# Optimization experiments

Measured on AMD Instinct MI355X. Metric: run time of the kernel, lower is better.

Reference implementation:

```python
import jax, jax.numpy as jnp
import numpy as np

D = 9  # nodefeat_n1 = 3 (resnet feat) + 6 (pos)


def _lstm_scan(x, Wih, Whh, bih, bhh, reverse=False):
    # x: [T, B, D] -> hidden states [T, B, D]; torch gate order i,f,g,o
    B = x.shape[1]
    def step(carry, xt):
        h, c = carry
        g = xt @ Wih.T + bih + h @ Whh.T + bhh
        i = jax.nn.sigmoid(g[:, :D])
        f = jax.nn.sigmoid(g[:, D:2*D])
        gg = jnp.tanh(g[:, 2*D:3*D])
        o = jax.nn.sigmoid(g[:, 3*D:])
        c = f * c + i * gg
        h = o * jnp.tanh(c)
        return (h, c), h
    init = (jnp.zeros((B, D), x.dtype), jnp.zeros((B, D), x.dtype))
    _, hs = jax.lax.scan(step, init, x, reverse=reverse)
    return hs


def _forward(nodes_feature, pos, attmat, msg_W, msg_b, gru_Wih, gru_Whh, gru_bih, gru_bhh,
             ro1_W, ro1_b, ro2_W, ro2_b, lf_Wih, lf_Whh, lf_bih, lf_bhh,
             lb_Wih, lb_Whh, lb_bih, lb_bhh, lr1_W, lr1_b, lr2_W, lr2_b, num_rec):
    node_feat = jnp.concatenate([nodes_feature, pos], axis=-1)  # [N,T,M,D]
    N, T, M, _ = node_feat.shape
    # valid_node_num = num_rec[b, 0] in the original code
    valid = (jnp.arange(M)[None, :] < num_rec[:, 0:1]).astype(node_feat.dtype)  # [N,M]
    att = attmat * valid[:, None, None, :]  # zero out invalid source nodes q
    src = node_feat  # message sources (h_w)
    hv = node_feat   # GRU hidden (h_v)
    hidden = node_feat
    for _ in range(2):  # iterN = 2 message-passing rounds
        msg = src @ msg_W.T + msg_b                    # [N,T,M,D] message_fc
        m = jnp.einsum('btnq,btqd->btnd', att, msg)    # attention-weighted sum over q
        # single-step GRU cell (torch gate order r,z,n)
        gx = m @ gru_Wih.T + gru_bih
        gh = hv @ gru_Whh.T + gru_bhh
        r = jax.nn.sigmoid(gx[..., :D] + gh[..., :D])
        z = jax.nn.sigmoid(gx[..., D:2*D] + gh[..., D:2*D])
        n = jnp.tanh(gx[..., 2*D:] + r * gh[..., 2*D:])
        h_new = (1.0 - z) * n + z * hv
        hidden = h_new * valid[:, None, :, None]       # invalid nodes never updated -> stay zero
        src = hidden
        hv = hidden
    vmask = valid[:, None, :, None]
    # per-frame readout (pred_label0)
    p0 = jax.nn.relu(hidden @ ro1_W.T + ro1_b) @ ro2_W.T + ro2_b
    pred_label0 = p0 * vmask
    # bidirectional LSTM over time, batched over (batch, node)
    x = hidden.transpose(1, 0, 2, 3).reshape(T, N * M, D)  # [T, N*M, D]
    hf = _lstm_scan(x, lf_Wih, lf_Whh, lf_bih, lf_bhh, reverse=False)
    hb = _lstm_scan(x, lb_Wih, lb_Whh, lb_bih, lb_bhh, reverse=True)
    out = jnp.concatenate([hf, hb], axis=-1).reshape(T, N, M, 2 * D).transpose(1, 0, 2, 3)
    p = jax.nn.relu(out @ lr1_W.T + lr1_b) @ lr2_W.T + lr2_b
    pred_label = p * vmask
    return pred_label, pred_label0


def setup_inputs() -> dict:
    key = jax.random.key(0)
    ks = jax.random.split(key, 32)
    N, T, M = 8192, 20, 6
    def u(k, shape, fan_in):
        s = 1.0 / np.sqrt(fan_in).astype(np.float32)
        return jax.random.uniform(k, shape, jnp.float32, -s, s)
    return {
        "nodes_feature": jax.random.normal(ks[0], (N, T, M, 3), jnp.float32),
        "pos": jax.random.normal(ks[1], (N, T, M, 6), jnp.float32),
        "attmat": jax.random.uniform(ks[2], (N, T, M, M), jnp.float32),
        "msg_W": u(ks[3], (D, D), D), "msg_b": u(ks[4], (D,), D),
        "gru_Wih": u(ks[5], (3 * D, D), D), "gru_Whh": u(ks[6], (3 * D, D), D),
        "gru_bih": u(ks[7], (3 * D,), D), "gru_bhh": u(ks[8], (3 * D,), D),
        "ro1_W": u(ks[9], (D, D), D), "ro1_b": u(ks[10], (D,), D),
        "ro2_W": u(ks[11], (7, D), D), "ro2_b": u(ks[12], (7,), D),
        "lf_Wih": u(ks[13], (4 * D, D), D), "lf_Whh": u(ks[14], (4 * D, D), D),
        "lf_bih": u(ks[15], (4 * D,), D), "lf_bhh": u(ks[16], (4 * D,), D),
        "lb_Wih": u(ks[17], (4 * D, D), D), "lb_Whh": u(ks[18], (4 * D, D), D),
        "lb_bih": u(ks[19], (4 * D,), D), "lb_bhh": u(ks[20], (4 * D,), D),
        "lr1_W": u(ks[21], (D, 2 * D), 2 * D), "lr1_b": u(ks[22], (D,), 2 * D),
        "lr2_W": u(ks[23], (7, D), D), "lr2_b": u(ks[24], (7,), D),
        "num_rec": jax.random.randint(ks[25], (N, T), 1, M + 1),
    }


def reference(nodes_feature, pos, attmat, msg_W, msg_b, gru_Wih, gru_Whh, gru_bih, gru_bhh,
              ro1_W, ro1_b, ro2_W, ro2_b, lf_Wih, lf_Whh, lf_bih, lf_bhh,
              lb_Wih, lb_Whh, lb_bih, lb_bhh, lr1_W, lr1_b, lr2_W, lr2_b, num_rec):
    return _forward(nodes_feature, pos, attmat, msg_W, msg_b, gru_Wih, gru_Whh, gru_bih, gru_bhh,
                    ro1_W, ro1_b, ro2_W, ro2_b, lf_Wih, lf_Whh, lf_bih, lf_bhh,
                    lb_Wih, lb_Whh, lb_bih, lb_bhh, lr1_W, lr1_b, lr2_W, lr2_b, num_rec)
```

## Files before the change

kernel.cpp:

```cpp
#include <hip/hip_runtime.h>

#define N_    8192
#define T_    20
#define M_    6
#define D_    9
#define NM_   (N_*M_)
#define NT_   (N_*T_)
#define NTM7_ (N_*T_*M_*7)

#define LOG2E 1.44269504088896f

typedef __attribute__((ext_vector_type(2))) float v2f;

__device__ __forceinline__ float sigm(float x){
    return __builtin_amdgcn_rcpf(1.f + __builtin_amdgcn_exp2f(-LOG2E * x));
}
__device__ __forceinline__ float tanh_(float x){
    return fmaf(2.f, __builtin_amdgcn_rcpf(1.f + __builtin_amdgcn_exp2f(-2.f*LOG2E * x)), -1.f);
}
__device__ __forceinline__ float shfl_(float v, int src){ return __shfl(v, src, 64); }
__device__ __forceinline__ v2f splat(float s){ return (v2f){s, s}; }
__device__ __forceinline__ v2f shfl2(v2f v, int src){
    v2f r; r.x = __shfl(v.x, src, 64); r.y = __shfl(v.y, src, 64); return r;
}
__device__ __forceinline__ v2f sigm2(v2f x){ v2f r; r.x = sigm(x.x); r.y = sigm(x.y); return r; }
__device__ __forceinline__ v2f tanh2(v2f x){ v2f r; r.x = tanh_(x.x); r.y = tanh_(x.y); return r; }
__device__ __forceinline__ v2f relu2(v2f x){ v2f r; r.x = fmaxf(x.x,0.f); r.y = fmaxf(x.y,0.f); return r; }

__global__ __launch_bounds__(256) void k_gnn(
    const float* __restrict__ nf,
    const float* __restrict__ pos,
    const float* __restrict__ am,
    const float* __restrict__ msgW, const float* __restrict__ msgb,
    const float* __restrict__ gWih, const float* __restrict__ gWhh,
    const float* __restrict__ gbih, const float* __restrict__ gbhh,
    const float* __restrict__ ro1W, const float* __restrict__ ro1b,
    const float* __restrict__ ro2W, const float* __restrict__ ro2b,
    const int*   __restrict__ numrec,
    float* __restrict__ hid,
    float* __restrict__ out0)
{
    const int lane = threadIdx.x & 63;
    const int wib  = threadIdx.x >> 6;
    const int g    = lane / 6;
    const int i    = lane - g * 6;
    const int gbase = g * 6;
    const bool lactive = (lane < 60);

    const int wbase = (blockIdx.x * 4 + wib) * 20;
    const int ntA = wbase + g;
    const int ntB = wbase + 10 + g;
    const int nA = ntA / T_, tA = ntA - nA * T_;
    const int nB = ntB / T_, tB = ntB - nB * T_;

    v2f s[D_];
    {
        const float* pA = nf + (size_t)ntA * 18 + i * 3;
        const float* pB = nf + (size_t)ntB * 18 + i * 3;
        #pragma unroll
        for (int k = 0; k < 3; ++k) { s[k].x = pA[k]; s[k].y = pB[k]; }
    }
    {
        const float* pA = pos + (size_t)ntA * 36 + i * 6;
        const float* pB = pos + (size_t)ntB * 36 + i * 6;
        #pragma unroll
        for (int k = 0; k < 6; ++k) { s[3+k].x = pA[k]; s[3+k].y = pB[k]; }
    }
    v2f attr[M_];
    {
        const float* pA = am + (size_t)ntA * 36 + i * 6;
        const float* pB = am + (size_t)ntB * 36 + i * 6;
        #pragma unroll
        for (int q = 0; q < M_; ++q) { attr[q].x = pA[q]; attr[q].y = pB[q]; }
    }
    const int nrA = numrec[nA * T_];
    const int nrB = numrec[nB * T_];
    #pragma unroll
    for (int q = 0; q < M_; ++q) {
        attr[q].x *= (q < nrA) ? 1.f : 0.f;
        attr[q].y *= (q < nrB) ? 1.f : 0.f;
    }
    v2f vmi; vmi.x = (i < nrA) ? 1.f : 0.f; vmi.y = (i < nrB) ? 1.f : 0.f;

    #pragma unroll
    for (int it = 0; it < 2; ++it) {
        v2f msg[D_];
        #pragma unroll
        for (int d = 0; d < D_; ++d) {
            v2f a = splat(msgb[d]);
            #pragma unroll
            for (int k = 0; k < D_; ++k) a += s[k] * msgW[d*9 + k];
            msg[d] = a;
        }
        v2f mm[D_];
        #pragma unroll
        for (int d = 0; d < D_; ++d) {
            v2f a = splat(0.f);
            #pragma unroll
            for (int q = 0; q < M_; ++q) a += attr[q] * shfl2(msg[d], gbase + q);
            mm[d] = a;
        }
        v2f grz[18], gxn[9], ghn[9];
        #pragma unroll
        for (int j = 0; j < 18; ++j) {
            v2f a = splat(gbih[j] + gbhh[j]);
            #pragma unroll
            for (int k = 0; k < D_; ++k) {
                a += mm[k] * gWih[j*9 + k];
                a += s[k]  * gWhh[j*9 + k];
            }
            grz[j] = a;
        }
        #pragma unroll
        for (int j = 0; j < 9; ++j) {
            v2f ax = splat(gbih[18 + j]), ah = splat(gbhh[18 + j]);
            #pragma unroll
            for (int k = 0; k < D_; ++k) {
                ax += mm[k] * gWih[(18 + j)*9 + k];
                ah += s[k]  * gWhh[(18 + j)*9 + k];
            }
            gxn[j] = ax; ghn[j] = ah;
        }
        #pragma unroll
        for (int d = 0; d < D_; ++d) {
            v2f r  = sigm2(grz[d]);
            v2f z  = sigm2(grz[9 + d]);
            v2f nn = tanh2(gxn[d] + r * ghn[d]);
            s[d] = vmi * ((splat(1.f) - z) * nn + z * s[d]);
        }
    }

    if (lactive) {
        float* hpA = hid + (size_t)(nA * M_ + i) * (T_ * D_) + tA * D_;
        float* hpB = hid + (size_t)(nB * M_ + i) * (T_ * D_) + tB * D_;
        #pragma unroll
        for (int d = 0; d < D_; ++d) { hpA[d] = s[d].x; hpB[d] = s[d].y; }
    }

    v2f q9[D_];
    #pragma unroll
    for (int d = 0; d < D_; ++d) {
        v2f a = splat(ro1b[d]);
        #pragma unroll
        for (int k = 0; k < D_; ++k) a += s[k] * ro1W[d*9 + k];
        q9[d] = relu2(a);
    }
    if (lactive) {
        float* opA = out0 + (size_t)ntA * 42 + i * 7;
        float* opB = out0 + (size_t)ntB * 42 + i * 7;
        #pragma unroll
        for (int j = 0; j < 7; ++j) {
            v2f a = splat(ro2b[j]);
            #pragma unroll
            for (int k = 0; k < D_; ++k) a += q9[k] * ro2W[j*9 + k];
            a *= vmi;
            opA[j] = a.x; opB[j] = a.y;
        }
    }
}

#define CPB 14

__global__ __launch_bounds__(128) void k_lstm(
    const float* __restrict__ hid,
    const float* __restrict__ fWih, const float* __restrict__ fWhh,
    const float* __restrict__ fbih, const float* __restrict__ fbhh,
    const float* __restrict__ bWih, const float* __restrict__ bWhh,
    const float* __restrict__ bbih, const float* __restrict__ bbhh,
    const float* __restrict__ lr1W, const float* __restrict__ lr1b,
    const float* __restrict__ lr2W, const float* __restrict__ lr2b,
    const int*   __restrict__ numrec,
    float* __restrict__ out)
{
    __shared__ float hst[16 * 404];
    __shared__ float hxs[16 * 20];

    const int lane = threadIdx.x & 63;
    const int wib  = threadIdx.x >> 6;
    const int grp0 = lane / 9;
    const int d    = lane - grp0 * 9;
    const int row  = wib * 8 + grp0;
    const int grp  = (grp0 < 7) ? grp0 : 6;

    bool active = (lane < 63);
    int ci = blockIdx.x * CPB + wib * 7 + grp;
    active = active && (ci < NM_);
    const int nm = active ? ci : 0;

    const float* xb = hid + (size_t)nm * (T_ * D_);
    const int crow = row * 20;
    const int hrow = row * 404;

    {
        float wxi[9], wxf[9], wxg[9], wxo[9], whi[9], whf[9], whg[9], who[9];
        #pragma unroll
        for (int k = 0; k < 9; ++k) {
            wxi[k] = fWih[(d     )*9 + k];  whi[k] = fWhh[(d     )*9 + k];
            wxf[k] = fWih[(9  + d)*9 + k];  whf[k] = fWhh[(9  + d)*9 + k];
            wxg[k] = fWih[(18 + d)*9 + k];  whg[k] = fWhh[(18 + d)*9 + k];
            wxo[k] = fWih[(27 + d)*9 + k];  who[k] = fWhh[(27 + d)*9 + k];
        }
        const float bi = fbih[d]      + fbhh[d];
        const float bf = fbih[9 + d]  + fbhh[9 + d];
        const float bg = fbih[18 + d] + fbhh[18 + d];
        const float bo = fbih[27 + d] + fbhh[27 + d];

        hxs[crow + 2*d] = 0.f;
        float h = 0.f, c = 0.f;
        for (int t = 0; t < T_; ++t) {
            hxs[crow + 2*d + 1] = xb[t*9 + d];
            float gi = bi, gf = bf, gg = bg, go = bo;
            #pragma unroll
            for (int j = 0; j < 8; j += 2) {
                float4 v = *(const float4*)&hxs[crow + 2*j];
                gi = fmaf(v.x, whi[j], fmaf(v.y, wxi[j], gi));
                gf = fmaf(v.x, whf[j], fmaf(v.y, wxf[j], gf));
                gg = fmaf(v.x, whg[j], fmaf(v.y, wxg[j], gg));
                go = fmaf(v.x, who[j], fmaf(v.y, wxo[j], go));
                gi = fmaf(v.z, whi[j+1], fmaf(v.w, wxi[j+1], gi));
                gf = fmaf(v.z, whf[j+1], fmaf(v.w, wxf[j+1], gf));
                gg = fmaf(v.z, whg[j+1], fmaf(v.w, wxg[j+1], gg));
                go = fmaf(v.z, who[j+1], fmaf(v.w, wxo[j+1], go));
            }
            {
                float2 v = *(const float2*)&hxs[crow + 16];
                gi = fmaf(v.x, whi[8], fmaf(v.y, wxi[8], gi));
                gf = fmaf(v.x, whf[8], fmaf(v.y, wxf[8], gf));
                gg = fmaf(v.x, whg[8], fmaf(v.y, wxg[8], gg));
                go = fmaf(v.x, who[8], fmaf(v.y, wxo[8], go));
            }
            c = sigm(gf) * c + sigm(gi) * tanh_(gg);
            h = sigm(go) * tanh_(c);
            hst[hrow + t*20 + d] = h;
            hxs[crow + 2*d] = h;
        }
    }

    {
        float wxi[9], wxf[9], wxg[9], wxo[9], whi[9], whf[9], whg[9], who[9];
        #pragma unroll
        for (int k = 0; k < 9; ++k) {
            wxi[k] = bWih[(d     )*9 + k];  whi[k] = bWhh[(d     )*9 + k];
            wxf[k] = bWih[(9  + d)*9 + k];  whf[k] = bWhh[(9  + d)*9 + k];
            wxg[k] = bWih[(18 + d)*9 + k];  whg[k] = bWhh[(18 + d)*9 + k];
            wxo[k] = bWih[(27 + d)*9 + k];  who[k] = bWhh[(27 + d)*9 + k];
        }
        const float bi = bbih[d]      + bbhh[d];
        const float bf = bbih[9 + d]  + bbhh[9 + d];
        const float bg = bbih[18 + d] + bbhh[18 + d];
        const float bo = bbih[27 + d] + bbhh[27 + d];

        hxs[crow + 2*d] = 0.f;
        float h = 0.f, c = 0.f;
        for (int tt = T_ - 1; tt >= 0; --tt) {
            hxs[crow + 2*d + 1] = xb[tt*9 + d];
            float gi = bi, gf = bf, gg = bg, go = bo;
            #pragma unroll
            for (int j = 0; j < 8; j += 2) {
                float4 v = *(const float4*)&hxs[crow + 2*j];
                gi = fmaf(v.x, whi[j], fmaf(v.y, wxi[j], gi));
                gf = fmaf(v.x, whf[j], fmaf(v.y, wxf[j], gf));
                gg = fmaf(v.x, whg[j], fmaf(v.y, wxg[j], gg));
                go = fmaf(v.x, who[j], fmaf(v.y, wxo[j], go));
                gi = fmaf(v.z, whi[j+1], fmaf(v.w, wxi[j+1], gi));
                gf = fmaf(v.z, whf[j+1], fmaf(v.w, wxf[j+1], gf));
                gg = fmaf(v.z, whg[j+1], fmaf(v.w, wxg[j+1], gg));
                go = fmaf(v.z, who[j+1], fmaf(v.w, wxo[j+1], go));
            }
            {
                float2 v = *(const float2*)&hxs[crow + 16];
                gi = fmaf(v.x, whi[8], fmaf(v.y, wxi[8], gi));
                gf = fmaf(v.x, whf[8], fmaf(v.y, wxf[8], gf));
                gg = fmaf(v.x, whg[8], fmaf(v.y, wxg[8], gg));
                go = fmaf(v.x, who[8], fmaf(v.y, wxo[8], go));
            }
            c = sigm(gf) * c + sigm(gi) * tanh_(gg);
            h = sigm(go) * tanh_(c);
            hst[hrow + tt*20 + 10 + d] = h;
            hxs[crow + 2*d] = h;
        }
    }

    #pragma unroll 1
    for (int rr = 0; rr < 3; ++rr) {
        const int item = rr * 64 + lane;
        if (item >= 140) break;
        const int ch = item / 20;
        const int t  = item - ch * 20;
        const int ci2 = blockIdx.x * CPB + wib * 7 + ch;
        if (ci2 >= NM_) continue;
        const int base = (wib * 8 + ch) * 404 + t * 20;

        float hf[9], hb[9];
        #pragma unroll
        for (int j = 0; j < 4; ++j) {
            float2 a = *(const float2*)&hst[base + 2*j];
            hf[2*j] = a.x; hf[2*j+1] = a.y;
            float2 b = *(const float2*)&hst[base + 10 + 2*j];
            hb[2*j] = b.x; hb[2*j+1] = b.y;
        }
        hf[8] = hst[base + 8];
        hb[8] = hst[base + 18];

        const int n2 = ci2 / M_;
        const int m2 = ci2 - n2 * M_;
        const float vi = (m2 < numrec[n2 * T_]) ? 1.f : 0.f;

        float q[9];
        #pragma unroll
        for (int dd = 0; dd < 9; ++dd) {
            float a = lr1b[dd];
            #pragma unroll
            for (int k = 0; k < 9; ++k) a = fmaf(hf[k], lr1W[dd*18 + k], a);
            #pragma unroll
            for (int k = 0; k < 9; ++k) a = fmaf(hb[k], lr1W[dd*18 + 9 + k], a);
            q[dd] = fmaxf(a, 0.f);
        }
        float* op = out + (size_t)((n2 * T_ + t) * M_ + m2) * 7;
        #pragma unroll
        for (int j = 0; j < 7; ++j) {
            float a = lr2b[j];
            #pragma unroll
            for (int k = 0; k < 9; ++k) a = fmaf(q[k], lr2W[j*9 + k], a);
            op[j] = a * vi;
        }
    }
}

extern "C" void kernel_launch(void* const* d_in, const int* in_sizes, int n_in,
                              void* d_out, int out_size, void* d_ws, size_t ws_size,
                              hipStream_t stream) {
    const float* nf    = (const float*)d_in[0];
    const float* pos   = (const float*)d_in[1];
    const float* am    = (const float*)d_in[2];
    const float* msgW  = (const float*)d_in[3];
    const float* msgb  = (const float*)d_in[4];
    const float* gWih  = (const float*)d_in[5];
    const float* gWhh  = (const float*)d_in[6];
    const float* gbih  = (const float*)d_in[7];
    const float* gbhh  = (const float*)d_in[8];
    const float* ro1W  = (const float*)d_in[9];
    const float* ro1b  = (const float*)d_in[10];
    const float* ro2W  = (const float*)d_in[11];
    const float* ro2b  = (const float*)d_in[12];
    const float* lfWih = (const float*)d_in[13];
    const float* lfWhh = (const float*)d_in[14];
    const float* lfbih = (const float*)d_in[15];
    const float* lfbhh = (const float*)d_in[16];
    const float* lbWih = (const float*)d_in[17];
    const float* lbWhh = (const float*)d_in[18];
    const float* lbbih = (const float*)d_in[19];
    const float* lbbhh = (const float*)d_in[20];
    const float* lr1W  = (const float*)d_in[21];
    const float* lr1b  = (const float*)d_in[22];
    const float* lr2W  = (const float*)d_in[23];
    const float* lr2b  = (const float*)d_in[24];
    const int* numrec  = (const int*)d_in[25];

    float* hid = (float*)d_ws;

    float* outp = (float*)d_out;
    float* out0 = (float*)d_out + NTM7_;

    k_gnn <<<NT_ / 80, 256, 0, stream>>>(nf, pos, am, msgW, msgb, gWih, gWhh,
                                         gbih, gbhh, ro1W, ro1b, ro2W, ro2b,
                                         numrec, hid, out0);
    const int lgrid = (NM_ + CPB - 1) / CPB;
    k_lstm<<<lgrid, 128, 0, stream>>>(hid, lfWih, lfWhh, lfbih, lfbhh,
                                      lbWih, lbWhh, lbbih, lbbhh,
                                      lr1W, lr1b, lr2W, lr2b, numrec, outp);
}
```

Measured before the change: 323.2 us.

## Exchange GNN messages via LDS instead of wave shuffles, one-wave blocks

Messages are now written to a shared-memory buffer and read back as float4 rows, where each lane used to gather neighbour messages with 12 cross-lane shuffles per feature. Blocks shrink to a single wave, so no block-level barrier is needed, and the grid is enlarged to keep the same coverage. The pos and attention loads are widened to float2, and the inactive lanes 60-63 are clamped to index 0. The aim is to replace many ds_bpermute operations with a few LDS writes and vector reads, at the cost of LDS traffic and smaller blocks.

```diff
diff --git a/kernel.cpp b/kernel.cpp
--- a/kernel.cpp
+++ b/kernel.cpp
@@ -18,16 +18,12 @@
 __device__ __forceinline__ float tanh_(float x){
     return fmaf(2.f, __builtin_amdgcn_rcpf(1.f + __builtin_amdgcn_exp2f(-2.f*LOG2E * x)), -1.f);
 }
-__device__ __forceinline__ float shfl_(float v, int src){ return __shfl(v, src, 64); }
 __device__ __forceinline__ v2f splat(float s){ return (v2f){s, s}; }
-__device__ __forceinline__ v2f shfl2(v2f v, int src){
-    v2f r; r.x = __shfl(v.x, src, 64); r.y = __shfl(v.y, src, 64); return r;
-}
 __device__ __forceinline__ v2f sigm2(v2f x){ v2f r; r.x = sigm(x.x); r.y = sigm(x.y); return r; }
 __device__ __forceinline__ v2f tanh2(v2f x){ v2f r; r.x = tanh_(x.x); r.y = tanh_(x.y); return r; }
 __device__ __forceinline__ v2f relu2(v2f x){ v2f r; r.x = fmaxf(x.x,0.f); r.y = fmaxf(x.y,0.f); return r; }
 
-__global__ __launch_bounds__(256) void k_gnn(
+__global__ __launch_bounds__(64) void k_gnn(
     const float* __restrict__ nf,
     const float* __restrict__ pos,
     const float* __restrict__ am,
@@ -40,16 +36,17 @@
     float* __restrict__ hid,
     float* __restrict__ out0)
 {
+    __shared__ v2f mbuf[11 * 58];
+
     const int lane = threadIdx.x & 63;
-    const int wib  = threadIdx.x >> 6;
     const int g    = lane / 6;
     const int i    = lane - g * 6;
-    const int gbase = g * 6;
+    const int gB   = g * 58;
     const bool lactive = (lane < 60);
 
-    const int wbase = (blockIdx.x * 4 + wib) * 20;
-    const int ntA = wbase + g;
-    const int ntB = wbase + 10 + g;
+    const int wbase = blockIdx.x * 20;
+    const int ntA = lactive ? (wbase + g)      : 0;
+    const int ntB = lactive ? (wbase + 10 + g) : 0;
     const int nA = ntA / T_, tA = ntA - nA * T_;
     const int nB = ntB / T_, tB = ntB - nB * T_;
 
@@ -61,17 +58,25 @@
         for (int k = 0; k < 3; ++k) { s[k].x = pA[k]; s[k].y = pB[k]; }
     }
     {
-        const float* pA = pos + (size_t)ntA * 36 + i * 6;
-        const float* pB = pos + (size_t)ntB * 36 + i * 6;
-        #pragma unroll
-        for (int k = 0; k < 6; ++k) { s[3+k].x = pA[k]; s[3+k].y = pB[k]; }
+        const float2* pA = (const float2*)(pos + (size_t)ntA * 36 + i * 6);
+        const float2* pB = (const float2*)(pos + (size_t)ntB * 36 + i * 6);
+        #pragma unroll
+        for (int k = 0; k < 3; ++k) {
+            float2 a = pA[k], b = pB[k];
+            s[3 + 2*k]     = (v2f){a.x, b.x};
+            s[3 + 2*k + 1] = (v2f){a.y, b.y};
+        }
     }
     v2f attr[M_];
     {
-        const float* pA = am + (size_t)ntA * 36 + i * 6;
-        const float* pB = am + (size_t)ntB * 36 + i * 6;
-        #pragma unroll
-        for (int q = 0; q < M_; ++q) { attr[q].x = pA[q]; attr[q].y = pB[q]; }
+        const float2* pA = (const float2*)(am + (size_t)ntA * 36 + i * 6);
+        const float2* pB = (const float2*)(am + (size_t)ntB * 36 + i * 6);
+        #pragma unroll
+        for (int k = 0; k < 3; ++k) {
+            float2 a = pA[k], b = pB[k];
+            attr[2*k]     = (v2f){a.x, b.x};
+            attr[2*k + 1] = (v2f){a.y, b.y};
+        }
     }
     const int nrA = numrec[nA * T_];
     const int nrB = numrec[nB * T_];
@@ -84,20 +89,24 @@
 
     #pragma unroll
     for (int it = 0; it < 2; ++it) {
-        v2f msg[D_];
         #pragma unroll
         for (int d = 0; d < D_; ++d) {
             v2f a = splat(msgb[d]);
             #pragma unroll
             for (int k = 0; k < D_; ++k) a += s[k] * msgW[d*9 + k];
-            msg[d] = a;
+            mbuf[gB + d*6 + i] = a;
         }
         v2f mm[D_];
         #pragma unroll
         for (int d = 0; d < D_; ++d) {
-            v2f a = splat(0.f);
-            #pragma unroll
-            for (int q = 0; q < M_; ++q) a += attr[q] * shfl2(msg[d], gbase + q);
+            const float4* rp = (const float4*)&mbuf[gB + d*6];
+            float4 p0 = rp[0], p1 = rp[1], p2 = rp[2];
+            v2f a = attr[0] * (v2f){p0.x, p0.y};
+            a += attr[1] * (v2f){p0.z, p0.w};
+            a += attr[2] * (v2f){p1.x, p1.y};
+            a += attr[3] * (v2f){p1.z, p1.w};
+            a += attr[4] * (v2f){p2.x, p2.y};
+            a += attr[5] * (v2f){p2.z, p2.w};
             mm[d] = a;
         }
         v2f grz[18], gxn[9], ghn[9];
@@ -362,9 +371,9 @@
     float* outp = (float*)d_out;
     float* out0 = (float*)d_out + NTM7_;
 
-    k_gnn <<<NT_ / 80, 256, 0, stream>>>(nf, pos, am, msgW, msgb, gWih, gWhh,
-                                         gbih, gbhh, ro1W, ro1b, ro2W, ro2b,
-                                         numrec, hid, out0);
+    k_gnn <<<NT_ / 20, 64, 0, stream>>>(nf, pos, am, msgW, msgb, gWih, gWhh,
+                                        gbih, gbhh, ro1W, ro1b, ro2W, ro2b,
+                                        numrec, hid, out0);
     const int lgrid = (NM_ + CPB - 1) / CPB;
     k_lstm<<<lgrid, 128, 0, stream>>>(hid, lfWih, lfWhh, lfbih, lfbhh,
                                       lbWih, lbWhh, lbbih, lbbhh,
```

New measurement: 291.5 us. -9.8%, faster.
